# Kernel tuning notes

Hardware: AMD Instinct MI355X
Metric: run time of the kernel (lower is better)

The kernel has to match this reference:

```python
import jax, jax.numpy as jnp
import numpy as np

GRID_SIZE = 3
LN_EPS = 1e-5
BASIS_EPS = 1e-6


def setup_inputs() -> dict:
    key = jax.random.key(0)
    ks = jax.random.split(key, 5)
    B, S, D_IN, D_OUT, SE_H = 8, 1024, 1024, 1024, 32
    x = jax.random.normal(ks[0], (B, S, D_IN), dtype=jnp.float32)
    base_weight = jax.random.normal(ks[1], (D_OUT, D_IN), dtype=jnp.float32) * 0.01
    spline_weight = jax.random.normal(ks[2], (D_OUT, D_IN, GRID_SIZE), dtype=jnp.float32) * 0.005
    ln_w = jnp.ones((D_OUT,), dtype=jnp.float32)
    ln_b = jnp.zeros((D_OUT,), dtype=jnp.float32)
    se_w1 = jax.random.normal(ks[3], (SE_H, D_OUT), dtype=jnp.float32) * 0.03
    se_b1 = jnp.zeros((SE_H,), dtype=jnp.float32)
    se_w2 = jax.random.normal(ks[4], (D_OUT, SE_H), dtype=jnp.float32) * 0.03
    se_b2 = jnp.zeros((D_OUT,), dtype=jnp.float32)
    return {"x": x, "base_weight": base_weight, "spline_weight": spline_weight,
            "ln_w": ln_w, "ln_b": ln_b, "se_w1": se_w1, "se_b1": se_b1,
            "se_w2": se_w2, "se_b2": se_b2}


def _kan_layer(x2d, base_weight, spline_weight, ln_w, ln_b, se_w1, se_b1, se_w2, se_b2):
    # x2d: [N, D_in]
    base = x2d @ base_weight.T                                   # [N, D_out]
    grid = jnp.linspace(-1.0, 1.0, GRID_SIZE).astype(x2d.dtype)  # [G]
    dist = jnp.abs(x2d[..., None] - grid)                        # [N, D_in, G]
    basis = jnp.where(dist < 1.0, (1.0 - dist) ** 2, 0.0)
    basis = basis / (basis.sum(axis=-1, keepdims=True) + BASIS_EPS)
    spline = jnp.einsum('nig,oig->no', basis, spline_weight)     # [N, D_out]
    out = base + spline
    # LayerNorm (dropout is identity at inference)
    mu = out.mean(axis=-1, keepdims=True)
    var = ((out - mu) ** 2).mean(axis=-1, keepdims=True)
    out = (out - mu) * jax.lax.rsqrt(var + LN_EPS) * ln_w + ln_b
    # SE gating (2D branch: applied per flattened token)
    h = jnp.maximum(out @ se_w1.T + se_b1, 0.0)
    se = jax.nn.sigmoid(h @ se_w2.T + se_b2)
    return out * se


def reference(x, base_weight, spline_weight, ln_w, ln_b, se_w1, se_b1, se_w2, se_b2):
    B, S, D = x.shape
    out = _kan_layer(x.reshape(-1, D), base_weight, spline_weight,
                     ln_w, ln_b, se_w1, se_b1, se_w2, se_b2)
    return out.reshape(B, S, -1)
```

## Files before the change

kernel.cpp:

```cpp
#include <hip/hip_runtime.h>
#include <hip/hip_bf16.h>
#include <math.h>

typedef __attribute__((ext_vector_type(8))) __bf16 bf16x8;
typedef __attribute__((ext_vector_type(4))) float f32x4;

#define NTOK 8192
#define DIN 1024
#define DOUT 1024
#define KAUG 4096
#define SEH 32

#define BK 64
#define KHALF 2048
#define NKT (KHALF / BK)

static __device__ __forceinline__ unsigned short f2bf(float f) {
  union { float f; unsigned u; } v; v.f = f;
  unsigned r = (v.u + 0x7FFFu + ((v.u >> 16) & 1u)) >> 16;
  return (unsigned short)r;
}

__global__ __launch_bounds__(256) void build_aaug(const float* __restrict__ x,
                                                  ushort* __restrict__ Aaug) {
  const int id = blockIdx.x * 256 + threadIdx.x;
  const float v = x[id];
  const float d0 = fabsf(v + 1.f), d1 = fabsf(v), d2 = fabsf(v - 1.f);
  float b0 = (d0 < 1.f) ? (1.f - d0) * (1.f - d0) : 0.f;
  float b1 = (d1 < 1.f) ? (1.f - d1) * (1.f - d1) : 0.f;
  float b2 = (d2 < 1.f) ? (1.f - d2) * (1.f - d2) : 0.f;
  const float inv = 1.f / (b0 + b1 + b2 + 1e-6f);
  ushort4 o;
  o.x = f2bf(v);
  o.y = f2bf(b0 * inv);
  o.z = f2bf(b1 * inv);
  o.w = f2bf(b2 * inv);
  ((ushort4*)Aaug)[id] = o;
}

__global__ __launch_bounds__(256) void pack_w(const float* __restrict__ bw,
                                              const float* __restrict__ sw,
                                              ushort* __restrict__ Waug) {
  const int id = blockIdx.x * 256 + threadIdx.x;
  ushort4 o;
  o.x = f2bf(bw[id]);
  o.y = f2bf(sw[id * 3 + 0]);
  o.z = f2bf(sw[id * 3 + 1]);
  o.w = f2bf(sw[id * 3 + 2]);
  ((ushort4*)Waug)[id] = o;
}

__global__ __launch_bounds__(256) void pack_se(const float* __restrict__ w1,
                                               const float* __restrict__ w2,
                                               ushort* __restrict__ w1b,
                                               ushort* __restrict__ w2b) {
  const int id = blockIdx.x * 256 + threadIdx.x;
  if (id < SEH * DOUT) w1b[id] = f2bf(w1[id]);
  else w2b[id - SEH * DOUT] = f2bf(w2[id - SEH * DOUT]);
}

#define WAITVM(N) asm volatile("s_waitcnt vmcnt(" #N ")" ::: "memory")

__global__ __launch_bounds__(512, 2) void gemm_sk(const ushort* __restrict__ A,
                                                  const ushort* __restrict__ B,
                                                  float* __restrict__ P0,
                                                  float* __restrict__ P1) {
  __shared__ ushort As[2][256 * BK];
  __shared__ ushort Bs[2][256 * BK];
  const int tid = threadIdx.x;
  const int wid = tid >> 6, lane = tid & 63;
  const int l16 = lane & 15, lk = lane >> 4;
  const int wm = wid >> 2, wn = wid & 3;

  const int g = (blockIdx.x & 7) * 32 + (blockIdx.x >> 3);
  const int kh = g >> 7;
  const int bm = (g & 127) >> 2;
  const int bn = g & 3;

  const ushort* Ab = A + (size_t)bm * 256 * KAUG + kh * KHALF;
  const ushort* Bb = B + (size_t)bn * 256 * KAUG + kh * KHALF;
  float* P = kh ? P1 : P0;

  const int lrow = lane >> 3;
  const int lcb = (lane & 7) ^ lrow;

  f32x4 acc[8][4] = {};

#define STAGE_A(kt, buf, r)                                                     \
  __builtin_amdgcn_global_load_lds(                                             \
      (const __attribute__((address_space(1))) void*)(Ab +                      \
          (size_t)((r) * 64 + wid * 8 + lrow) * KAUG + (kt) * BK + lcb * 8),    \
      (__attribute__((address_space(3))) void*)(&As[buf][((r) * 512 + wid * 64) * 8]), \
      16, 0, 0)
#define STAGE_B(kt, buf, r)                                                     \
  __builtin_amdgcn_global_load_lds(                                             \
      (const __attribute__((address_space(1))) void*)(Bb +                      \
          (size_t)((r) * 64 + wid * 8 + lrow) * KAUG + (kt) * BK + lcb * 8),    \
      (__attribute__((address_space(3))) void*)(&Bs[buf][((r) * 512 + wid * 64) * 8]), \
      16, 0, 0)
#define STAGE_ALL(kt, buf)                                                      \
  do {                                                                          \
    STAGE_A(kt, buf, 0); STAGE_A(kt, buf, 1); STAGE_A(kt, buf, 2); STAGE_A(kt, buf, 3); \
    STAGE_B(kt, buf, 0); STAGE_B(kt, buf, 1); STAGE_B(kt, buf, 2); STAGE_B(kt, buf, 3); \
  } while (0)

#define RD_A(buf, m, kk) \
  (*(const bf16x8*)&As[buf][(wm * 128 + (m) * 16 + l16) * 64 + ((((kk) * 4 + lk) ^ (l16 & 7)) << 3)])
#define RD_B(buf, n, kk) \
  (*(const bf16x8*)&Bs[buf][(wn * 64 + (n) * 16 + l16) * 64 + ((((kk) * 4 + lk) ^ (l16 & 7)) << 3)])

  STAGE_ALL(0, 0);

  int bc = 0;
  for (int kt = 0; kt < NKT; ++kt) {
    if (kt < NKT - 1) {
      STAGE_ALL(kt + 1, bc ^ 1);
      WAITVM(8);
    } else {
      WAITVM(0);
    }
    __builtin_amdgcn_s_barrier();
    __builtin_amdgcn_sched_barrier(0);

    bf16x8 af[8][2], bfr[4][2];
#pragma unroll
    for (int m = 0; m < 8; ++m) { af[m][0] = RD_A(bc, m, 0); af[m][1] = RD_A(bc, m, 1); }
#pragma unroll
    for (int n = 0; n < 4; ++n) { bfr[n][0] = RD_B(bc, n, 0); bfr[n][1] = RD_B(bc, n, 1); }

    __builtin_amdgcn_s_setprio(1);
#pragma unroll
    for (int k2 = 0; k2 < 2; ++k2)
#pragma unroll
      for (int m = 0; m < 8; ++m)
#pragma unroll
        for (int n = 0; n < 4; ++n)
          acc[m][n] = __builtin_amdgcn_mfma_f32_16x16x32_bf16(af[m][k2], bfr[n][k2], acc[m][n], 0, 0, 0);
    __builtin_amdgcn_s_setprio(0);

    __builtin_amdgcn_s_barrier();
    bc ^= 1;
  }

  float* Cb = P + (size_t)(bm * 256 + wm * 128) * DOUT + bn * 256 + wn * 64;
#pragma unroll
  for (int m = 0; m < 8; ++m)
#pragma unroll
    for (int n = 0; n < 4; ++n)
#pragma unroll
      for (int j = 0; j < 4; ++j)
        Cb[(size_t)(m * 16 + lk * 4 + j) * DOUT + n * 16 + l16] = acc[m][n][j];
}

__global__ __launch_bounds__(256) void ln_se_mfma(
    float* __restrict__ out, const float* __restrict__ p1,
    const float* __restrict__ ln_w, const float* __restrict__ ln_b,
    const ushort* __restrict__ w1b, const float* __restrict__ se_b1,
    const ushort* __restrict__ w2b, const float* __restrict__ se_b2) {
  __shared__ float Yl[16 * 1028];
  __shared__ float Hpart[4][512];
  __shared__ unsigned Hb[256];
  const int tid = threadIdx.x;
  const int w = tid >> 6, lane = tid & 63;
  const int l16 = lane & 15, lk = lane >> 4;
  const int tok0 = blockIdx.x * 16;

  float lw[16], lb[16];
#pragma unroll
  for (int e = 0; e < 16; ++e) {
    lw[e] = ln_w[e * 64 + lane];
    lb[e] = ln_b[e * 64 + lane];
  }

  for (int q = 0; q < 4; ++q) {
    const int tl = w * 4 + q;
    const float* r0 = out + (size_t)(tok0 + tl) * DOUT;
    const float* r1 = p1 + (size_t)(tok0 + tl) * DOUT;
    float v[16];
#pragma unroll
    for (int e = 0; e < 16; ++e) v[e] = r0[e * 64 + lane] + r1[e * 64 + lane];
    float s = 0.f, ss = 0.f;
#pragma unroll
    for (int e = 0; e < 16; ++e) { s += v[e]; ss += v[e] * v[e]; }
#pragma unroll
    for (int m = 32; m; m >>= 1) { s += __shfl_xor(s, m); ss += __shfl_xor(ss, m); }
    const float mu = s * (1.f / (float)DOUT);
    const float inv = rsqrtf(ss * (1.f / (float)DOUT) - mu * mu + 1e-5f);
#pragma unroll
    for (int e = 0; e < 16; ++e)
      Yl[tl * 1028 + e * 64 + lane] = (v[e] - mu) * inv * lw[e] + lb[e];
  }
  __syncthreads();

  f32x4 acc1[2] = {};
#pragma unroll
  for (int s = 0; s < 8; ++s) {
    const int ks = w * 8 + s;
    const int k = ks * 32 + lk * 8;
    const float* yp = &Yl[l16 * 1028 + k];
    const f32x4 q0 = *(const f32x4*)yp;
    const f32x4 q1 = *(const f32x4*)(yp + 4);
    bf16x8 af;
    af[0] = (__bf16)q0[0]; af[1] = (__bf16)q0[1];
    af[2] = (__bf16)q0[2]; af[3] = (__bf16)q0[3];
    af[4] = (__bf16)q1[0]; af[5] = (__bf16)q1[1];
    af[6] = (__bf16)q1[2]; af[7] = (__bf16)q1[3];
#pragma unroll
    for (int nt = 0; nt < 2; ++nt) {
      const bf16x8 bf = *(const bf16x8*)(w1b + (nt * 16 + l16) * 1024 + ks * 32 + lk * 8);
      acc1[nt] = __builtin_amdgcn_mfma_f32_16x16x32_bf16(af, bf, acc1[nt], 0, 0, 0);
    }
  }
#pragma unroll
  for (int nt = 0; nt < 2; ++nt)
#pragma unroll
    for (int j = 0; j < 4; ++j)
      Hpart[w][(lk * 4 + j) * 32 + nt * 16 + l16] = acc1[nt][j];
  __syncthreads();

  {
    const int e2 = tid * 2;
    float h0 = Hpart[0][e2] + Hpart[1][e2] + Hpart[2][e2] + Hpart[3][e2];
    float h1 = Hpart[0][e2 + 1] + Hpart[1][e2 + 1] + Hpart[2][e2 + 1] + Hpart[3][e2 + 1];
    h0 = fmaxf(h0 + se_b1[e2 & 31], 0.f);
    h1 = fmaxf(h1 + se_b1[(e2 & 31) + 1], 0.f);
    Hb[tid] = (unsigned)f2bf(h0) | ((unsigned)f2bf(h1) << 16);
  }
  __syncthreads();

  union { uint4 u; bf16x8 v; } ha;
  ha.u = *(const uint4*)&Hb[l16 * 16 + lk * 4];
  const int nbase = w * 256;
#pragma unroll
  for (int nt = 0; nt < 16; ++nt) {
    const int col = nbase + nt * 16 + l16;
    const bf16x8 bf = *(const bf16x8*)(w2b + col * 32 + lk * 8);
    f32x4 gz = {0.f, 0.f, 0.f, 0.f};
    gz = __builtin_amdgcn_mfma_f32_16x16x32_bf16(ha.v, bf, gz, 0, 0, 0);
    const float b2 = se_b2[col];
#pragma unroll
    for (int j = 0; j < 4; ++j) {
      const int tl = lk * 4 + j;
      const float sg = 1.f / (1.f + __expf(-(gz[j] + b2)));
      out[(size_t)(tok0 + tl) * DOUT + col] = Yl[tl * 1028 + col] * sg;
    }
  }
}

extern "C" void kernel_launch(void* const* d_in, const int* in_sizes, int n_in,
                              void* d_out, int out_size, void* d_ws, size_t ws_size,
                              hipStream_t stream) {
  const float* x = (const float*)d_in[0];
  const float* bw = (const float*)d_in[1];
  const float* sw = (const float*)d_in[2];
  const float* ln_w = (const float*)d_in[3];
  const float* ln_b = (const float*)d_in[4];
  const float* se_w1 = (const float*)d_in[5];
  const float* se_b1 = (const float*)d_in[6];
  const float* se_w2 = (const float*)d_in[7];
  const float* se_b2 = (const float*)d_in[8];
  float* out = (float*)d_out;

  ushort* Aaug = (ushort*)d_ws;
  ushort* Waug = Aaug + (size_t)NTOK * KAUG;
  ushort* w1b = Waug + (size_t)DOUT * KAUG;
  ushort* w2b = w1b + SEH * DOUT;
  float* P1 = (float*)(w2b + SEH * DOUT);

  build_aaug<<<NTOK * DIN / 256, 256, 0, stream>>>(x, Aaug);
  pack_w<<<DOUT * DIN / 256, 256, 0, stream>>>(bw, sw, Waug);
  pack_se<<<2 * SEH * DOUT / 256, 256, 0, stream>>>(se_w1, se_w2, w1b, w2b);
  gemm_sk<<<256, 512, 0, stream>>>(Aaug, Waug, out, P1);
  ln_se_mfma<<<NTOK / 16, 256, 0, stream>>>(out, P1, ln_w, ln_b, w1b, se_b1, w2b, se_b2);
}
```

Measured before the change: 120.0 us.

## Fuse prep kernels, store split-K partials as bf16, precompute LDS swizzle offsets

Merges the three packing kernels into one launch. The GEMM now writes both split-K partials in bf16 to workspace instead of fp32, which halves partial-store and reload traffic, and the LN/SE kernel reads both bf16 partials with packed loads. The GEMM main loop is unrolled by two with a fixed buffer index, and the swizzled LDS read offsets are hoisted out of the loop. Rounding each partial to bf16 before summing adds precision loss.

```diff
diff --git a/kernel.cpp b/kernel.cpp
--- a/kernel.cpp
+++ b/kernel.cpp
@@ -20,51 +20,58 @@
   unsigned r = (v.u + 0x7FFFu + ((v.u >> 16) & 1u)) >> 16;
   return (unsigned short)r;
 }
-
-__global__ __launch_bounds__(256) void build_aaug(const float* __restrict__ x,
-                                                  ushort* __restrict__ Aaug) {
-  const int id = blockIdx.x * 256 + threadIdx.x;
-  const float v = x[id];
-  const float d0 = fabsf(v + 1.f), d1 = fabsf(v), d2 = fabsf(v - 1.f);
-  float b0 = (d0 < 1.f) ? (1.f - d0) * (1.f - d0) : 0.f;
-  float b1 = (d1 < 1.f) ? (1.f - d1) * (1.f - d1) : 0.f;
-  float b2 = (d2 < 1.f) ? (1.f - d2) * (1.f - d2) : 0.f;
-  const float inv = 1.f / (b0 + b1 + b2 + 1e-6f);
-  ushort4 o;
-  o.x = f2bf(v);
-  o.y = f2bf(b0 * inv);
-  o.z = f2bf(b1 * inv);
-  o.w = f2bf(b2 * inv);
-  ((ushort4*)Aaug)[id] = o;
-}
-
-__global__ __launch_bounds__(256) void pack_w(const float* __restrict__ bw,
-                                              const float* __restrict__ sw,
-                                              ushort* __restrict__ Waug) {
-  const int id = blockIdx.x * 256 + threadIdx.x;
-  ushort4 o;
-  o.x = f2bf(bw[id]);
-  o.y = f2bf(sw[id * 3 + 0]);
-  o.z = f2bf(sw[id * 3 + 1]);
-  o.w = f2bf(sw[id * 3 + 2]);
-  ((ushort4*)Waug)[id] = o;
-}
-
-__global__ __launch_bounds__(256) void pack_se(const float* __restrict__ w1,
-                                               const float* __restrict__ w2,
-                                               ushort* __restrict__ w1b,
-                                               ushort* __restrict__ w2b) {
-  const int id = blockIdx.x * 256 + threadIdx.x;
-  if (id < SEH * DOUT) w1b[id] = f2bf(w1[id]);
-  else w2b[id - SEH * DOUT] = f2bf(w2[id - SEH * DOUT]);
+static __device__ __forceinline__ float bflo(unsigned u) {
+  union { unsigned u; float f; } v; v.u = u << 16; return v.f;
+}
+static __device__ __forceinline__ float bfhi(unsigned u) {
+  union { unsigned u; float f; } v; v.u = u & 0xFFFF0000u; return v.f;
+}
+
+__global__ __launch_bounds__(256) void prep(const float* __restrict__ x,
+                                            const float* __restrict__ bw,
+                                            const float* __restrict__ sw,
+                                            const float* __restrict__ w1,
+                                            const float* __restrict__ w2,
+                                            ushort* __restrict__ Aaug,
+                                            ushort* __restrict__ Waug,
+                                            ushort* __restrict__ w1b,
+                                            ushort* __restrict__ w2b) {
+  const int b = blockIdx.x;
+  if (b < 32768) {
+    const int id = b * 256 + threadIdx.x;
+    const float v = x[id];
+    const float d0 = fabsf(v + 1.f), d1 = fabsf(v), d2 = fabsf(v - 1.f);
+    float b0 = (d0 < 1.f) ? (1.f - d0) * (1.f - d0) : 0.f;
+    float b1 = (d1 < 1.f) ? (1.f - d1) * (1.f - d1) : 0.f;
+    float b2 = (d2 < 1.f) ? (1.f - d2) * (1.f - d2) : 0.f;
+    const float inv = 1.f / (b0 + b1 + b2 + 1e-6f);
+    ushort4 o;
+    o.x = f2bf(v);
+    o.y = f2bf(b0 * inv);
+    o.z = f2bf(b1 * inv);
+    o.w = f2bf(b2 * inv);
+    ((ushort4*)Aaug)[id] = o;
+  } else if (b < 32768 + 4096) {
+    const int id = (b - 32768) * 256 + threadIdx.x;
+    ushort4 o;
+    o.x = f2bf(bw[id]);
+    o.y = f2bf(sw[id * 3 + 0]);
+    o.z = f2bf(sw[id * 3 + 1]);
+    o.w = f2bf(sw[id * 3 + 2]);
+    ((ushort4*)Waug)[id] = o;
+  } else {
+    const int id = (b - 32768 - 4096) * 256 + threadIdx.x;
+    if (id < SEH * DOUT) w1b[id] = f2bf(w1[id]);
+    else w2b[id - SEH * DOUT] = f2bf(w2[id - SEH * DOUT]);
+  }
 }
 
 #define WAITVM(N) asm volatile("s_waitcnt vmcnt(" #N ")" ::: "memory")
 
 __global__ __launch_bounds__(512, 2) void gemm_sk(const ushort* __restrict__ A,
                                                   const ushort* __restrict__ B,
-                                                  float* __restrict__ P0,
-                                                  float* __restrict__ P1) {
+                                                  ushort* __restrict__ P0,
+                                                  ushort* __restrict__ P1) {
   __shared__ ushort As[2][256 * BK];
   __shared__ ushort Bs[2][256 * BK];
   const int tid = threadIdx.x;
@@ -79,10 +86,15 @@
 
   const ushort* Ab = A + (size_t)bm * 256 * KAUG + kh * KHALF;
   const ushort* Bb = B + (size_t)bn * 256 * KAUG + kh * KHALF;
-  float* P = kh ? P1 : P0;
+  ushort* P = kh ? P1 : P0;
 
   const int lrow = lane >> 3;
   const int lcb = (lane & 7) ^ lrow;
+
+  const int aBase = (wm * 128 + l16) * 64;
+  const int bBase = (wn * 64 + l16) * 64;
+  const int sw0 = ((l16 & 4) << 3) + ((lk ^ (l16 & 3)) << 3);
+  const int sw1 = sw0 ^ 32;
 
   f32x4 acc[8][4] = {};
 
@@ -104,56 +116,60 @@
     STAGE_B(kt, buf, 0); STAGE_B(kt, buf, 1); STAGE_B(kt, buf, 2); STAGE_B(kt, buf, 3); \
   } while (0)
 
-#define RD_A(buf, m, kk) \
-  (*(const bf16x8*)&As[buf][(wm * 128 + (m) * 16 + l16) * 64 + ((((kk) * 4 + lk) ^ (l16 & 7)) << 3)])
-#define RD_B(buf, n, kk) \
-  (*(const bf16x8*)&Bs[buf][(wn * 64 + (n) * 16 + l16) * 64 + ((((kk) * 4 + lk) ^ (l16 & 7)) << 3)])
+#define TILE(kt, CB, NB)                                                        \
+  do {                                                                          \
+    if ((kt) < NKT - 1) {                                                       \
+      STAGE_ALL((kt) + 1, NB);                                                  \
+      WAITVM(8);                                                                \
+    } else {                                                                    \
+      WAITVM(0);                                                                \
+    }                                                                           \
+    __builtin_amdgcn_s_barrier();                                               \
+    __builtin_amdgcn_sched_barrier(0);                                          \
+    bf16x8 af[8][2], bfr[4][2];                                                 \
+    _Pragma("unroll")                                                           \
+    for (int m = 0; m < 8; ++m) {                                               \
+      af[m][0] = *(const bf16x8*)&As[CB][aBase + m * 1024 + sw0];               \
+      af[m][1] = *(const bf16x8*)&As[CB][aBase + m * 1024 + sw1];               \
+    }                                                                           \
+    _Pragma("unroll")                                                           \
+    for (int n = 0; n < 4; ++n) {                                               \
+      bfr[n][0] = *(const bf16x8*)&Bs[CB][bBase + n * 1024 + sw0];              \
+      bfr[n][1] = *(const bf16x8*)&Bs[CB][bBase + n * 1024 + sw1];              \
+    }                                                                           \
+    __builtin_amdgcn_s_setprio(1);                                              \
+    _Pragma("unroll")                                                           \
+    for (int k2 = 0; k2 < 2; ++k2)                                              \
+      _Pragma("unroll")                                                         \
+      for (int m = 0; m < 8; ++m)                                               \
+        _Pragma("unroll")                                                       \
+        for (int n = 0; n < 4; ++n)                                             \
+          acc[m][n] = __builtin_amdgcn_mfma_f32_16x16x32_bf16(                  \
+              af[m][k2], bfr[n][k2], acc[m][n], 0, 0, 0);                       \
+    __builtin_amdgcn_s_setprio(0);                                              \
+    __builtin_amdgcn_s_barrier();                                               \
+  } while (0)
 
   STAGE_ALL(0, 0);
 
-  int bc = 0;
-  for (int kt = 0; kt < NKT; ++kt) {
-    if (kt < NKT - 1) {
-      STAGE_ALL(kt + 1, bc ^ 1);
-      WAITVM(8);
-    } else {
-      WAITVM(0);
-    }
-    __builtin_amdgcn_s_barrier();
-    __builtin_amdgcn_sched_barrier(0);
-
-    bf16x8 af[8][2], bfr[4][2];
-#pragma unroll
-    for (int m = 0; m < 8; ++m) { af[m][0] = RD_A(bc, m, 0); af[m][1] = RD_A(bc, m, 1); }
-#pragma unroll
-    for (int n = 0; n < 4; ++n) { bfr[n][0] = RD_B(bc, n, 0); bfr[n][1] = RD_B(bc, n, 1); }
-
-    __builtin_amdgcn_s_setprio(1);
-#pragma unroll
-    for (int k2 = 0; k2 < 2; ++k2)
-#pragma unroll
-      for (int m = 0; m < 8; ++m)
-#pragma unroll
-        for (int n = 0; n < 4; ++n)
-          acc[m][n] = __builtin_amdgcn_mfma_f32_16x16x32_bf16(af[m][k2], bfr[n][k2], acc[m][n], 0, 0, 0);
-    __builtin_amdgcn_s_setprio(0);
-
-    __builtin_amdgcn_s_barrier();
-    bc ^= 1;
-  }
-
-  float* Cb = P + (size_t)(bm * 256 + wm * 128) * DOUT + bn * 256 + wn * 64;
+  for (int kt2 = 0; kt2 < NKT; kt2 += 2) {
+    TILE(kt2, 0, 1);
+    TILE(kt2 + 1, 1, 0);
+  }
+
+  ushort* Cb = P + (size_t)(bm * 256 + wm * 128) * DOUT + bn * 256 + wn * 64;
 #pragma unroll
   for (int m = 0; m < 8; ++m)
 #pragma unroll
     for (int n = 0; n < 4; ++n)
 #pragma unroll
       for (int j = 0; j < 4; ++j)
-        Cb[(size_t)(m * 16 + lk * 4 + j) * DOUT + n * 16 + l16] = acc[m][n][j];
+        Cb[(size_t)(m * 16 + lk * 4 + j) * DOUT + n * 16 + l16] = f2bf(acc[m][n][j]);
 }
 
 __global__ __launch_bounds__(256) void ln_se_mfma(
-    float* __restrict__ out, const float* __restrict__ p1,
+    float* __restrict__ out,
+    const ushort* __restrict__ p0, const ushort* __restrict__ p1,
     const float* __restrict__ ln_w, const float* __restrict__ ln_b,
     const ushort* __restrict__ w1b, const float* __restrict__ se_b1,
     const ushort* __restrict__ w2b, const float* __restrict__ se_b2) {
@@ -165,30 +181,41 @@
   const int l16 = lane & 15, lk = lane >> 4;
   const int tok0 = blockIdx.x * 16;
 
-  float lw[16], lb[16];
-#pragma unroll
-  for (int e = 0; e < 16; ++e) {
-    lw[e] = ln_w[e * 64 + lane];
-    lb[e] = ln_b[e * 64 + lane];
-  }
-
-  for (int q = 0; q < 4; ++q) {
-    const int tl = w * 4 + q;
-    const float* r0 = out + (size_t)(tok0 + tl) * DOUT;
-    const float* r1 = p1 + (size_t)(tok0 + tl) * DOUT;
-    float v[16];
-#pragma unroll
-    for (int e = 0; e < 16; ++e) v[e] = r0[e * 64 + lane] + r1[e * 64 + lane];
+  float2 lwp[8], lbp[8];
+#pragma unroll
+  for (int q = 0; q < 8; ++q) {
+    lwp[q] = ((const float2*)ln_w)[q * 64 + lane];
+    lbp[q] = ((const float2*)ln_b)[q * 64 + lane];
+  }
+
+  for (int qt = 0; qt < 4; ++qt) {
+    const int tl = w * 4 + qt;
+    const uint* r0 = (const uint*)(p0 + (size_t)(tok0 + tl) * DOUT);
+    const uint* r1 = (const uint*)(p1 + (size_t)(tok0 + tl) * DOUT);
+    float v0[8], v1[8];
+#pragma unroll
+    for (int q = 0; q < 8; ++q) {
+      const uint a = r0[q * 64 + lane], b = r1[q * 64 + lane];
+      v0[q] = bflo(a) + bflo(b);
+      v1[q] = bfhi(a) + bfhi(b);
+    }
     float s = 0.f, ss = 0.f;
 #pragma unroll
-    for (int e = 0; e < 16; ++e) { s += v[e]; ss += v[e] * v[e]; }
+    for (int q = 0; q < 8; ++q) {
+      s += v0[q] + v1[q];
+      ss += v0[q] * v0[q] + v1[q] * v1[q];
+    }
 #pragma unroll
     for (int m = 32; m; m >>= 1) { s += __shfl_xor(s, m); ss += __shfl_xor(ss, m); }
     const float mu = s * (1.f / (float)DOUT);
     const float inv = rsqrtf(ss * (1.f / (float)DOUT) - mu * mu + 1e-5f);
 #pragma unroll
-    for (int e = 0; e < 16; ++e)
-      Yl[tl * 1028 + e * 64 + lane] = (v[e] - mu) * inv * lw[e] + lb[e];
+    for (int q = 0; q < 8; ++q) {
+      float2 y2;
+      y2.x = (v0[q] - mu) * inv * lwp[q].x + lbp[q].x;
+      y2.y = (v1[q] - mu) * inv * lwp[q].y + lbp[q].y;
+      *(float2*)&Yl[tl * 1028 + (q * 64 + lane) * 2] = y2;
+    }
   }
   __syncthreads();
 
@@ -265,11 +292,12 @@
   ushort* Waug = Aaug + (size_t)NTOK * KAUG;
   ushort* w1b = Waug + (size_t)DOUT * KAUG;
   ushort* w2b = w1b + SEH * DOUT;
-  float* P1 = (float*)(w2b + SEH * DOUT);
-
-  build_aaug<<<NTOK * DIN / 256, 256, 0, stream>>>(x, Aaug);
-  pack_w<<<DOUT * DIN / 256, 256, 0, stream>>>(bw, sw, Waug);
-  pack_se<<<2 * SEH * DOUT / 256, 256, 0, stream>>>(se_w1, se_w2, w1b, w2b);
-  gemm_sk<<<256, 512, 0, stream>>>(Aaug, Waug, out, P1);
-  ln_se_mfma<<<NTOK / 16, 256, 0, stream>>>(out, P1, ln_w, ln_b, w1b, se_b1, w2b, se_b2);
-}
+  ushort* P0b = w2b + SEH * DOUT;
+  ushort* P1b = P0b + (size_t)NTOK * DOUT;
+
+  prep<<<32768 + 4096 + 256, 256, 0, stream>>>(x, bw, sw, se_w1, se_w2,
+                                               Aaug, Waug, w1b, w2b);
+  gemm_sk<<<256, 512, 0, stream>>>(Aaug, Waug, P0b, P1b);
+  ln_se_mfma<<<NTOK / 16, 256, 0, stream>>>(out, P0b, P1b, ln_w, ln_b,
+                                            w1b, se_b1, w2b, se_b2);
+}
```

New measurement: 138.3 us. +15.3%, slower.
